# Optimization experiments

Measured on AMD Instinct MI355X. Metric: run time of the kernel, lower is better.

The kernel has to match this reference:

```python
import jax, jax.numpy as jnp
import numpy as np

N_HEADS = 16

def _rope(x):
    # x: (B, T, H, D); rotary embedding over sequence positions T
    B, T, H, D = x.shape
    half = D // 2
    freqs = 1.0 / (10000.0 ** (jnp.arange(half, dtype=x.dtype) / half))
    t = jnp.arange(T, dtype=x.dtype)
    ang = t[:, None] * freqs[None, :]            # (T, half)
    cos = jnp.cos(ang)[:, None, :]               # (T, 1, half) broadcast over heads
    sin = jnp.sin(ang)[:, None, :]
    x1, x2 = x[..., :half], x[..., half:]
    return jnp.concatenate([x1 * cos - x2 * sin, x1 * sin + x2 * cos], axis=-1)


def setup_inputs() -> dict:
    key = jax.random.key(0)
    kx, kq, kk, kv, ko = jax.random.split(key, 5)
    B, T, C = 4, 2048, 2048
    x = jax.random.normal(kx, (B, T, C), dtype=jnp.float32)
    # TPLinear (tp_size=1): weight (out_f, in_f), init randn*0.02, no bias
    wq = jax.random.normal(kq, (C, C), dtype=jnp.float32) * 0.02
    wk = jax.random.normal(kk, (C, C), dtype=jnp.float32) * 0.02
    wv = jax.random.normal(kv, (C, C), dtype=jnp.float32) * 0.02
    wo = jax.random.normal(ko, (C, C), dtype=jnp.float32) * 0.02
    return {"x": x, "wq": wq, "wk": wk, "wv": wv, "wo": wo}


def reference(x, wq, wk, wv, wo):
    B, T, C = x.shape
    H = N_HEADS
    D = C // H
    # QKV projections (F.linear: x @ W^T)
    q = (x @ wq.T).reshape(B, T, H, D)
    k = (x @ wk.T).reshape(B, T, H, D)
    v = (x @ wv.T).reshape(B, T, H, D)
    # RoPE on q and k over sequence positions
    q = _rope(q).transpose(0, 2, 1, 3)           # (B, H, T, D)
    k = _rope(k).transpose(0, 2, 1, 3)
    v = v.transpose(0, 2, 1, 3)
    # Causal scaled dot-product attention
    scale = 1.0 / jnp.sqrt(jnp.asarray(D, dtype=x.dtype))
    scores = jnp.einsum("bhqd,bhkd->bhqk", q, k) * scale   # (B, H, T, T)
    causal = jnp.tril(jnp.ones((T, T), dtype=bool))
    scores = jnp.where(causal, scores, jnp.finfo(x.dtype).min)
    att = jax.nn.softmax(scores, axis=-1)
    out = jnp.einsum("bhqk,bhkd->bhqd", att, v)            # (B, H, T, D)
    out = out.transpose(0, 2, 1, 3).reshape(B, T, C)
    return out @ wo.T
```

## Files before the change

kernel.cpp:

```cpp
#include <hip/hip_runtime.h>
#include <hip/hip_bf16.h>
#include <stdint.h>

typedef __hip_bfloat16 bf16;
typedef __bf16 bf16x8_t __attribute__((ext_vector_type(8)));
typedef float f32x4_t __attribute__((ext_vector_type(4)));

#define GAS __attribute__((address_space(1)))
#define LAS __attribute__((address_space(3)))

__device__ __forceinline__ f32x4_t mfma16(bf16x8_t a, bf16x8_t b, f32x4_t c) {
    return __builtin_amdgcn_mfma_f32_16x16x32_bf16(a, b, c, 0, 0, 0);
}

__device__ __forceinline__ void gload_lds16(const void* g, void* l) {
    __builtin_amdgcn_global_load_lds((const GAS void*)g, (LAS void*)l, 16, 0, 0);
}

__device__ __forceinline__ int swzK(int a) { return a ^ (((a >> 8) & 7) << 4); }
__device__ __forceinline__ int swzV(int a) { return a ^ (((a >> 7) & 7) << 4); }

__global__ __launch_bounds__(256) void cast_f32_bf16(const float* __restrict__ in,
                                                     bf16* __restrict__ out, int n4) {
    int stride = gridDim.x * blockDim.x;
    for (int i = blockIdx.x * blockDim.x + threadIdx.x; i < n4; i += stride) {
        float4 f = reinterpret_cast<const float4*>(in)[i];
        bf16 h0 = __float2bfloat16(f.x), h1 = __float2bfloat16(f.y);
        bf16 h2 = __float2bfloat16(f.z), h3 = __float2bfloat16(f.w);
        ushort4 u;
        u.x = *reinterpret_cast<unsigned short*>(&h0);
        u.y = *reinterpret_cast<unsigned short*>(&h1);
        u.z = *reinterpret_cast<unsigned short*>(&h2);
        u.w = *reinterpret_cast<unsigned short*>(&h3);
        reinterpret_cast<ushort4*>(out)[i] = u;
    }
}

__device__ __forceinline__ void store_out(float* p, float v) { *p = v; }
__device__ __forceinline__ void store_out(bf16* p, float v) { *p = __float2bfloat16(v); }

template <typename OutT>
__global__ __launch_bounds__(256) void gemm_nt(const bf16* __restrict__ A,
                                               const bf16* __restrict__ B,
                                               OutT* __restrict__ C,
                                               int M, int N, int K) {
    __shared__ bf16 As[128 * 32];
    __shared__ bf16 Bs[128 * 32];
    const int t = threadIdx.x;
    const int lane = t & 63;
    const int wv = t >> 6;
    const int wr = wv >> 1, wc = wv & 1;
    const int m0 = blockIdx.y * 128, n0 = blockIdx.x * 128;

    f32x4_t acc[4][4];
#pragma unroll
    for (int i = 0; i < 4; i++)
#pragma unroll
        for (int j = 0; j < 4; j++) acc[i][j] = f32x4_t{0.f, 0.f, 0.f, 0.f};

    const char* Ab = (const char*)A;
    const char* Bb = (const char*)B;
    const int srow = t >> 2;
    const int scolb = (t & 3) * 16;

    for (int k0 = 0; k0 < K; k0 += 32) {
#pragma unroll
        for (int i = 0; i < 2; ++i) {
            int row = i * 64 + srow;
            gload_lds16(Ab + ((size_t)(m0 + row) * K + k0) * 2 + scolb,
                        (char*)As + (i * 256 + wv * 64) * 16);
            gload_lds16(Bb + ((size_t)(n0 + row) * K + k0) * 2 + scolb,
                        (char*)Bs + (i * 256 + wv * 64) * 16);
        }
        __syncthreads();
        bf16x8_t af[4], bfb[4];
#pragma unroll
        for (int mi = 0; mi < 4; mi++)
            af[mi] = *reinterpret_cast<const bf16x8_t*>(
                (const char*)As + (wr * 64 + mi * 16 + (lane & 15)) * 64 + (lane >> 4) * 16);
#pragma unroll
        for (int ni = 0; ni < 4; ni++)
            bfb[ni] = *reinterpret_cast<const bf16x8_t*>(
                (const char*)Bs + (wc * 64 + ni * 16 + (lane & 15)) * 64 + (lane >> 4) * 16);
#pragma unroll
        for (int mi = 0; mi < 4; mi++)
#pragma unroll
            for (int ni = 0; ni < 4; ni++)
                acc[mi][ni] = mfma16(af[mi], bfb[ni], acc[mi][ni]);
        __syncthreads();
    }

#pragma unroll
    for (int mi = 0; mi < 4; mi++)
#pragma unroll
        for (int ni = 0; ni < 4; ni++)
#pragma unroll
            for (int r = 0; r < 4; r++) {
                int row = m0 + wr * 64 + mi * 16 + ((lane >> 4) << 2) + r;
                int col = n0 + wc * 64 + ni * 16 + (lane & 15);
                store_out(C + (size_t)row * N + col, acc[mi][ni][r]);
            }
}

__global__ __launch_bounds__(256) void rope_qk(bf16* __restrict__ q, bf16* __restrict__ k,
                                               int total) {
    int idx = blockIdx.x * blockDim.x + threadIdx.x;
    if (idx >= total) return;
    int d = idx & 63;
    int h = (idx >> 6) & 15;
    int bt = idx >> 10;
    int tpos = bt & 2047;
    float freq = expf(-0.14391157f * (float)d);
    float ang = (float)tpos * freq;
    float s, c;
    sincosf(ang, &s, &c);
    size_t base = (size_t)bt * 2048 + h * 128 + d;
    const float scale_q = 0.08838834764831845f;
    {
        float x1 = __bfloat162float(q[base]);
        float x2 = __bfloat162float(q[base + 64]);
        q[base]      = __float2bfloat16((x1 * c - x2 * s) * scale_q);
        q[base + 64] = __float2bfloat16((x1 * s + x2 * c) * scale_q);
    }
    {
        float x1 = __bfloat162float(k[base]);
        float x2 = __bfloat162float(k[base + 64]);
        k[base]      = __float2bfloat16(x1 * c - x2 * s);
        k[base + 64] = __float2bfloat16(x1 * s + x2 * c);
    }
}

__global__ __launch_bounds__(256) void transpose_v(const bf16* __restrict__ v,
                                                   bf16* __restrict__ vT) {
    __shared__ bf16 tile[64][65];
    const int T = 2048, Cc = 2048;
    int bh = blockIdx.z, b = bh >> 4, h = bh & 15;
    int t0 = blockIdx.x * 64, d0 = blockIdx.y * 64;
    int tx = threadIdx.x & 63, ty = threadIdx.x >> 6;
#pragma unroll
    for (int i = 0; i < 16; i++) {
        int tt = ty + i * 4;
        tile[tt][tx] = v[(size_t)(b * T + t0 + tt) * Cc + h * 128 + d0 + tx];
    }
    __syncthreads();
#pragma unroll
    for (int i = 0; i < 16; i++) {
        int dd = ty + i * 4;
        vT[(size_t)(bh * 128 + d0 + dd) * T + t0 + tx] = tile[tx][dd];
    }
}

__global__ __launch_bounds__(256) void flash_attn(const bf16* __restrict__ q,
                                                  const bf16* __restrict__ k,
                                                  const bf16* __restrict__ vT,
                                                  bf16* __restrict__ att) {
    const int T = 2048, Cc = 2048;
    __shared__ bf16 Ks[64 * 128];
    __shared__ bf16 VTs[128 * 64];
    __shared__ bf16 Ps[4][16 * 72];
    const int t = threadIdx.x, lane = t & 63, w = t >> 6;
    const int bh = blockIdx.y, b = bh >> 4, h = bh & 15;
    const int col = lane & 15, hi = lane >> 4;

    for (int pass = 0; pass < 2; ++pass) {
        const int qblk = pass ? (31 - (int)blockIdx.x) : (int)blockIdx.x;
        const int q0 = qblk * 64;

        bf16x8_t qf[4];
        {
            int qrow = q0 + w * 16 + col;
            const char* qb = (const char*)q + ((size_t)(b * T + qrow) * Cc + h * 128) * 2;
#pragma unroll
            for (int kf = 0; kf < 4; kf++)
                qf[kf] = *reinterpret_cast<const bf16x8_t*>(qb + kf * 64 + hi * 16);
        }

        f32x4_t acc[8];
#pragma unroll
        for (int i = 0; i < 8; i++) acc[i] = f32x4_t{0.f, 0.f, 0.f, 0.f};
        float m_run[4] = {-1e30f, -1e30f, -1e30f, -1e30f};
        float l_run[4] = {0.f, 0.f, 0.f, 0.f};

        const int ntiles = qblk + 1;
        for (int ti = 0; ti < ntiles; ++ti) {
            const int k0 = ti * 64;
#pragma unroll
            for (int i = 0; i < 4; ++i) {
                int o = (i * 256 + t) * 16;
                int kr = o >> 8, kc = (o & 255) ^ ((kr & 7) << 4);
                gload_lds16((const char*)k + ((size_t)(b * T + k0 + kr) * Cc + h * 128) * 2 + kc,
                            (char*)Ks + (i * 256 + w * 64) * 16);
                int vr = o >> 7, vc = (o & 127) ^ ((vr & 7) << 4);
                gload_lds16((const char*)vT + ((size_t)(bh * 128 + vr) * T + k0) * 2 + vc,
                            (char*)VTs + (i * 256 + w * 64) * 16);
            }
            __syncthreads();

            f32x4_t s[4];
#pragma unroll
            for (int nb = 0; nb < 4; nb++) {
                s[nb] = f32x4_t{0.f, 0.f, 0.f, 0.f};
#pragma unroll
                for (int kf = 0; kf < 4; kf++) {
                    bf16x8_t kfr = *reinterpret_cast<const bf16x8_t*>(
                        (const char*)Ks + swzK((nb * 16 + col) * 256 + kf * 64 + hi * 16));
                    s[nb] = mfma16(qf[kf], kfr, s[nb]);
                }
            }

            const int rowb = q0 + w * 16 + (hi << 2);
            float mt[4] = {-1e30f, -1e30f, -1e30f, -1e30f};
#pragma unroll
            for (int nb = 0; nb < 4; nb++) {
                int kc = k0 + nb * 16 + col;
#pragma unroll
                for (int r = 0; r < 4; r++) {
                    float v = s[nb][r];
                    if (kc > rowb + r) v = -1e30f;
                    s[nb][r] = v;
                    mt[r] = fmaxf(mt[r], v);
                }
            }
#pragma unroll
            for (int r = 0; r < 4; r++) {
#pragma unroll
                for (int mk = 1; mk < 16; mk <<= 1)
                    mt[r] = fmaxf(mt[r], __shfl_xor(mt[r], mk, 64));
            }
            float alpha[4], ls[4];
#pragma unroll
            for (int r = 0; r < 4; r++) {
                float mn = fmaxf(m_run[r], mt[r]);
                alpha[r] = __expf(m_run[r] - mn);
                m_run[r] = mn;
                ls[r] = 0.f;
            }
#pragma unroll
            for (int nb = 0; nb < 4; nb++)
#pragma unroll
                for (int r = 0; r < 4; r++) {
                    float p = __expf(s[nb][r] - m_run[r]);
                    s[nb][r] = p;
                    ls[r] += p;
                }
#pragma unroll
            for (int r = 0; r < 4; r++) {
#pragma unroll
                for (int mk = 1; mk < 16; mk <<= 1)
                    ls[r] += __shfl_xor(ls[r], mk, 64);
                l_run[r] = l_run[r] * alpha[r] + ls[r];
            }
#pragma unroll
            for (int i = 0; i < 8; i++)
#pragma unroll
                for (int r = 0; r < 4; r++) acc[i][r] *= alpha[r];

#pragma unroll
            for (int nb = 0; nb < 4; nb++)
#pragma unroll
                for (int r = 0; r < 4; r++)
                    Ps[w][((hi << 2) + r) * 72 + nb * 16 + col] =
                        __float2bfloat16(s[nb][r]);
            asm volatile("s_waitcnt lgkmcnt(0)" ::: "memory");
            __builtin_amdgcn_sched_barrier(0);
            bf16x8_t pf[2];
#pragma unroll
            for (int kb = 0; kb < 2; kb++)
                pf[kb] = *reinterpret_cast<const bf16x8_t*>(
                    (const char*)Ps[w] + col * 144 + kb * 64 + hi * 16);

#pragma unroll
            for (int db = 0; db < 8; db++)
#pragma unroll
                for (int kb = 0; kb < 2; kb++) {
                    bf16x8_t vf = *reinterpret_cast<const bf16x8_t*>(
                        (const char*)VTs + swzV((db * 16 + col) * 128 + kb * 64 + hi * 16));
                    acc[db] = mfma16(pf[kb], vf, acc[db]);
                }
            __syncthreads();
        }

#pragma unroll
        for (int r = 0; r < 4; r++) {
            float inv = 1.0f / l_run[r];
            int row = q0 + w * 16 + (hi << 2) + r;
            size_t base = (size_t)(b * T + row) * Cc + h * 128;
#pragma unroll
            for (int db = 0; db < 8; db++)
                att[base + db * 16 + col] = __float2bfloat16(acc[db][r] * inv);
        }
    }
}

extern "C" void kernel_launch(void* const* d_in, const int* in_sizes, int n_in,
                              void* d_out, int out_size, void* d_ws, size_t ws_size,
                              hipStream_t stream) {
    const int B = 4, T = 2048, C = 2048;
    const int M = B * T;
    const float* x  = (const float*)d_in[0];
    const float* wq = (const float*)d_in[1];
    const float* wk = (const float*)d_in[2];
    const float* wv = (const float*)d_in[3];
    const float* wo = (const float*)d_in[4];
    float* out = (float*)d_out;

    char* ws = (char*)d_ws;
    const size_t SZ_X = (size_t)M * C * 2;
    const size_t SZ_W = (size_t)C * C * 2;
    bf16* xb   = (bf16*)(ws);
    bf16* wqb  = (bf16*)(ws + SZ_X);
    bf16* wkb  = (bf16*)(ws + SZ_X + SZ_W);
    bf16* wvb  = (bf16*)(ws + SZ_X + 2 * SZ_W);
    bf16* wob  = (bf16*)(ws + SZ_X + 3 * SZ_W);
    bf16* qb   = (bf16*)(ws + SZ_X + 4 * SZ_W);
    bf16* kb   = (bf16*)(ws + 2 * SZ_X + 4 * SZ_W);
    bf16* vb   = (bf16*)(ws + 3 * SZ_X + 4 * SZ_W);
    bf16* vTb  = (bf16*)(ws + 4 * SZ_X + 4 * SZ_W);
    bf16* attb = (bf16*)(ws + 5 * SZ_X + 4 * SZ_W);

    cast_f32_bf16<<<2048, 256, 0, stream>>>(x, xb, M * C / 4);
    cast_f32_bf16<<<1024, 256, 0, stream>>>(wq, wqb, C * C / 4);
    cast_f32_bf16<<<1024, 256, 0, stream>>>(wk, wkb, C * C / 4);
    cast_f32_bf16<<<1024, 256, 0, stream>>>(wv, wvb, C * C / 4);
    cast_f32_bf16<<<1024, 256, 0, stream>>>(wo, wob, C * C / 4);

    dim3 ggrid(C / 128, M / 128);
    gemm_nt<bf16><<<ggrid, 256, 0, stream>>>(xb, wqb, qb, M, C, C);
    gemm_nt<bf16><<<ggrid, 256, 0, stream>>>(xb, wkb, kb, M, C, C);
    gemm_nt<bf16><<<ggrid, 256, 0, stream>>>(xb, wvb, vb, M, C, C);

    int rope_total = B * T * 16 * 64;
    rope_qk<<<rope_total / 256, 256, 0, stream>>>(qb, kb, rope_total);

    transpose_v<<<dim3(T / 64, 2, B * 16), 256, 0, stream>>>(vb, vTb);

    flash_attn<<<dim3(16, B * 16), 256, 0, stream>>>(qb, kb, vTb, attb);

    gemm_nt<float><<<ggrid, 256, 0, stream>>>(attb, wob, out, M, C, C);
}
```

Before: 817.2 us.

## Replace GEMM with 256x256 double-buffered swizzled kernel and use exp2 softmax

Replaces the 128x128 single-stage GEMM with a 256x256-tile, 512-thread kernel. It stages K=64 slices into two LDS buffers with XOR-swizzled layout, overlaps global loads with MFMA via explicit waitcnt and barriers, raises wave priority during MFMA, and remaps block indices for L2 locality. Attention folds log2(e) into the Q scale so softmax can use exp2f, and the K/V swizzle expressions are simplified. The GEMM uses 128KB of LDS at one block per CU, which reduces occupancy.

```diff
diff --git a/kernel.cpp b/kernel.cpp
--- a/kernel.cpp
+++ b/kernel.cpp
@@ -8,6 +8,7 @@
 
 #define GAS __attribute__((address_space(1)))
 #define LAS __attribute__((address_space(3)))
+#define SCHED0 __builtin_amdgcn_sched_barrier(0)
 
 __device__ __forceinline__ f32x4_t mfma16(bf16x8_t a, bf16x8_t b, f32x4_t c) {
     return __builtin_amdgcn_mfma_f32_16x16x32_bf16(a, b, c, 0, 0, 0);
@@ -16,9 +17,6 @@
 __device__ __forceinline__ void gload_lds16(const void* g, void* l) {
     __builtin_amdgcn_global_load_lds((const GAS void*)g, (LAS void*)l, 16, 0, 0);
 }
-
-__device__ __forceinline__ int swzK(int a) { return a ^ (((a >> 8) & 7) << 4); }
-__device__ __forceinline__ int swzV(int a) { return a ^ (((a >> 7) & 7) << 4); }
 
 __global__ __launch_bounds__(256) void cast_f32_bf16(const float* __restrict__ in,
                                                      bf16* __restrict__ out, int n4) {
@@ -40,65 +38,116 @@
 __device__ __forceinline__ void store_out(bf16* p, float v) { *p = __float2bfloat16(v); }
 
 template <typename OutT>
-__global__ __launch_bounds__(256) void gemm_nt(const bf16* __restrict__ A,
-                                               const bf16* __restrict__ B,
-                                               OutT* __restrict__ C,
-                                               int M, int N, int K) {
-    __shared__ bf16 As[128 * 32];
-    __shared__ bf16 Bs[128 * 32];
-    const int t = threadIdx.x;
-    const int lane = t & 63;
-    const int wv = t >> 6;
-    const int wr = wv >> 1, wc = wv & 1;
-    const int m0 = blockIdx.y * 128, n0 = blockIdx.x * 128;
-
-    f32x4_t acc[4][4];
-#pragma unroll
-    for (int i = 0; i < 4; i++)
-#pragma unroll
-        for (int j = 0; j < 4; j++) acc[i][j] = f32x4_t{0.f, 0.f, 0.f, 0.f};
-
-    const char* Ab = (const char*)A;
-    const char* Bb = (const char*)B;
-    const int srow = t >> 2;
-    const int scolb = (t & 3) * 16;
-
-    for (int k0 = 0; k0 < K; k0 += 32) {
-#pragma unroll
-        for (int i = 0; i < 2; ++i) {
-            int row = i * 64 + srow;
-            gload_lds16(Ab + ((size_t)(m0 + row) * K + k0) * 2 + scolb,
-                        (char*)As + (i * 256 + wv * 64) * 16);
-            gload_lds16(Bb + ((size_t)(n0 + row) * K + k0) * 2 + scolb,
-                        (char*)Bs + (i * 256 + wv * 64) * 16);
-        }
-        __syncthreads();
-        bf16x8_t af[4], bfb[4];
-#pragma unroll
-        for (int mi = 0; mi < 4; mi++)
-            af[mi] = *reinterpret_cast<const bf16x8_t*>(
-                (const char*)As + (wr * 64 + mi * 16 + (lane & 15)) * 64 + (lane >> 4) * 16);
-#pragma unroll
-        for (int ni = 0; ni < 4; ni++)
-            bfb[ni] = *reinterpret_cast<const bf16x8_t*>(
-                (const char*)Bs + (wc * 64 + ni * 16 + (lane & 15)) * 64 + (lane >> 4) * 16);
-#pragma unroll
-        for (int mi = 0; mi < 4; mi++)
-#pragma unroll
-            for (int ni = 0; ni < 4; ni++)
-                acc[mi][ni] = mfma16(af[mi], bfb[ni], acc[mi][ni]);
-        __syncthreads();
-    }
-
-#pragma unroll
-    for (int mi = 0; mi < 4; mi++)
-#pragma unroll
-        for (int ni = 0; ni < 4; ni++)
-#pragma unroll
-            for (int r = 0; r < 4; r++) {
-                int row = m0 + wr * 64 + mi * 16 + ((lane >> 4) << 2) + r;
-                int col = n0 + wc * 64 + ni * 16 + (lane & 15);
-                store_out(C + (size_t)row * N + col, acc[mi][ni][r]);
+__global__ __launch_bounds__(512, 1) void gemm_nt256(const bf16* __restrict__ A,
+                                                     const bf16* __restrict__ B,
+                                                     OutT* __restrict__ C,
+                                                     int M, int N, int K) {
+    __shared__ char lds[131072];
+    const int t = threadIdx.x, lane = t & 63, w = t >> 6;
+    const int wm = w >> 2, wn = w & 3;
+    const int li = lane & 15, hi = lane >> 4, l7 = lane & 7, l3 = lane >> 3;
+
+    const int ny = M >> 8;
+    const int cpx = gridDim.x >> 3;
+    const int tile = ((int)blockIdx.x & 7) * cpx + ((int)blockIdx.x >> 3);
+    const int m0 = (tile % ny) * 256, n0 = (tile / ny) * 256;
+    const int NT = K >> 6;
+
+    f32x4_t acc[8][4];
+#pragma unroll
+    for (int f = 0; f < 8; ++f)
+#pragma unroll
+        for (int g = 0; g < 4; ++g) acc[f][g] = f32x4_t{0.f, 0.f, 0.f, 0.f};
+
+    bf16x8_t af[2][8], bfr[2][4];
+
+    auto stage = [&](int kt, int p) {
+        const char* Ab = (const char*)A;
+        const char* Bb = (const char*)B;
+        char* la = lds + p * 65536;
+        char* lb = la + 32768;
+        const int sc = (l7 ^ l3) << 4;
+        const size_t kof = (size_t)kt * 128;
+#pragma unroll
+        for (int c = 0; c < 4; ++c) {
+            int row = w * 32 + c * 8 + l3;
+            gload_lds16(Ab + (size_t)(m0 + row) * K * 2 + kof + sc,
+                        la + (w * 32 + c * 8) * 128);
+        }
+#pragma unroll
+        for (int c = 0; c < 4; ++c) {
+            int row = w * 32 + c * 8 + l3;
+            gload_lds16(Bb + (size_t)(n0 + row) * K * 2 + kof + sc,
+                        lb + (w * 32 + c * 8) * 128);
+        }
+    };
+
+    auto read_frags = [&](int p) {
+        const char* la = lds + p * 65536;
+        const char* lb = la + 32768;
+#pragma unroll
+        for (int kk = 0; kk < 2; ++kk) {
+            const int cb = kk * 64 + hi * 16;
+#pragma unroll
+            for (int f = 0; f < 8; ++f) {
+                int r = wm * 128 + f * 16 + li;
+                af[kk][f] = *reinterpret_cast<const bf16x8_t*>(
+                    la + r * 128 + (cb ^ (l7 << 4)));
+            }
+#pragma unroll
+            for (int g = 0; g < 4; ++g) {
+                int r = wn * 64 + g * 16 + li;
+                bfr[kk][g] = *reinterpret_cast<const bf16x8_t*>(
+                    lb + r * 128 + (cb ^ (l7 << 4)));
+            }
+        }
+    };
+
+    auto do_mfma = [&]() {
+        __builtin_amdgcn_s_setprio(1);
+#pragma unroll
+        for (int kk = 0; kk < 2; ++kk)
+#pragma unroll
+            for (int f = 0; f < 8; ++f)
+#pragma unroll
+                for (int g = 0; g < 4; ++g)
+                    acc[f][g] = mfma16(af[kk][f], bfr[kk][g], acc[f][g]);
+        __builtin_amdgcn_s_setprio(0);
+    };
+
+    stage(0, 0);
+    stage(1, 1);
+    asm volatile("s_waitcnt vmcnt(8)" ::: "memory"); SCHED0;
+    __builtin_amdgcn_s_barrier(); SCHED0;
+
+    for (int kt = 0; kt < NT - 2; ++kt) {
+        const int p = kt & 1;
+        read_frags(p);
+        asm volatile("s_waitcnt lgkmcnt(0)" ::: "memory"); SCHED0;
+        __builtin_amdgcn_s_barrier(); SCHED0;
+        stage(kt + 2, p);
+        do_mfma();
+        asm volatile("s_waitcnt vmcnt(8)" ::: "memory"); SCHED0;
+        __builtin_amdgcn_s_barrier(); SCHED0;
+    }
+    read_frags((NT - 2) & 1);
+    asm volatile("s_waitcnt lgkmcnt(0)" ::: "memory"); SCHED0;
+    do_mfma();
+    asm volatile("s_waitcnt vmcnt(0)" ::: "memory"); SCHED0;
+    __builtin_amdgcn_s_barrier(); SCHED0;
+    read_frags((NT - 1) & 1);
+    asm volatile("s_waitcnt lgkmcnt(0)" ::: "memory"); SCHED0;
+    do_mfma();
+
+#pragma unroll
+    for (int f = 0; f < 8; ++f)
+#pragma unroll
+        for (int g = 0; g < 4; ++g)
+#pragma unroll
+            for (int r = 0; r < 4; ++r) {
+                int row = m0 + wm * 128 + f * 16 + hi * 4 + r;
+                int col = n0 + wn * 64 + g * 16 + li;
+                store_out(C + (size_t)row * N + col, acc[f][g][r]);
             }
 }
 
@@ -115,7 +164,7 @@
     float s, c;
     sincosf(ang, &s, &c);
     size_t base = (size_t)bt * 2048 + h * 128 + d;
-    const float scale_q = 0.08838834764831845f;
+    const float scale_q = 0.12751682f;
     {
         float x1 = __bfloat162float(q[base]);
         float x2 = __bfloat162float(q[base + 64]);
@@ -203,7 +252,8 @@
 #pragma unroll
                 for (int kf = 0; kf < 4; kf++) {
                     bf16x8_t kfr = *reinterpret_cast<const bf16x8_t*>(
-                        (const char*)Ks + swzK((nb * 16 + col) * 256 + kf * 64 + hi * 16));
+                        (const char*)Ks + (((nb * 16 + col) * 256 + kf * 64 + hi * 16)
+                                           ^ ((col & 7) << 4)));
                     s[nb] = mfma16(qf[kf], kfr, s[nb]);
                 }
             }
@@ -231,7 +281,7 @@
 #pragma unroll
             for (int r = 0; r < 4; r++) {
                 float mn = fmaxf(m_run[r], mt[r]);
-                alpha[r] = __expf(m_run[r] - mn);
+                alpha[r] = exp2f(m_run[r] - mn);
                 m_run[r] = mn;
                 ls[r] = 0.f;
             }
@@ -239,7 +289,7 @@
             for (int nb = 0; nb < 4; nb++)
 #pragma unroll
                 for (int r = 0; r < 4; r++) {
-                    float p = __expf(s[nb][r] - m_run[r]);
+                    float p = exp2f(s[nb][r] - m_run[r]);
                     s[nb][r] = p;
                     ls[r] += p;
                 }
@@ -274,7 +324,8 @@
 #pragma unroll
                 for (int kb = 0; kb < 2; kb++) {
                     bf16x8_t vf = *reinterpret_cast<const bf16x8_t*>(
-                        (const char*)VTs + swzV((db * 16 + col) * 128 + kb * 64 + hi * 16));
+                        (const char*)VTs + (((db * 16 + col) * 128 + kb * 64 + hi * 16)
+                                            ^ ((col & 7) << 4)));
                     acc[db] = mfma16(pf[kb], vf, acc[db]);
                 }
             __syncthreads();
@@ -324,10 +375,10 @@
     cast_f32_bf16<<<1024, 256, 0, stream>>>(wv, wvb, C * C / 4);
     cast_f32_bf16<<<1024, 256, 0, stream>>>(wo, wob, C * C / 4);
 
-    dim3 ggrid(C / 128, M / 128);
-    gemm_nt<bf16><<<ggrid, 256, 0, stream>>>(xb, wqb, qb, M, C, C);
-    gemm_nt<bf16><<<ggrid, 256, 0, stream>>>(xb, wkb, kb, M, C, C);
-    gemm_nt<bf16><<<ggrid, 256, 0, stream>>>(xb, wvb, vb, M, C, C);
+    const int nblk = (M / 256) * (C / 256);
+    gemm_nt256<bf16><<<nblk, 512, 0, stream>>>(xb, wqb, qb, M, C, C);
+    gemm_nt256<bf16><<<nblk, 512, 0, stream>>>(xb, wkb, kb, M, C, C);
+    gemm_nt256<bf16><<<nblk, 512, 0, stream>>>(xb, wvb, vb, M, C, C);
 
     int rope_total = B * T * 16 * 64;
     rope_qk<<<rope_total / 256, 256, 0, stream>>>(qb, kb, rope_total);
@@ -336,5 +387,5 @@
 
     flash_attn<<<dim3(16, B * 16), 256, 0, stream>>>(qb, kb, vTb, attb);
 
-    gemm_nt<float><<<ggrid, 256, 0, stream>>>(attb, wob, out, M, C, C);
-}
+    gemm_nt256<float><<<nblk, 512, 0, stream>>>(attb, wob, out, M, C, C);
+}
```

New measurement: 800.2 us. 1.02x faster.
